# Kernel optimization log

Hardware: AMD Instinct MI355X
Metric: run time of the kernel (lower is better)

The kernel has to match this reference:

```python
import jax, jax.numpy as jnp
import numpy as np

EPS = 1e-4

def _softmax_kernel(data, projection_matrix, is_query):
    # data: [..., n, d], projection_matrix: [m, d]
    d = data.shape[-1]
    m = projection_matrix.shape[0]
    data_normalizer = 1.0 / (d ** 0.25)
    ratio = 1.0 / (m ** 0.5)
    # [..., n, m]
    data_dash = jnp.einsum('...id,jd->...ij', data_normalizer * data, projection_matrix)
    # ||x||^2 / 2 * normalizer^2, shape [..., n, 1]
    diag_data = (jnp.sum(data * data, axis=-1) * 0.5 * data_normalizer ** 2)[..., None]
    if is_query:
        stab = jnp.max(data_dash, axis=-1, keepdims=True)
    else:
        stab = jnp.max(data_dash)
    return ratio * (jnp.exp(data_dash - diag_data - stab) + EPS)

def _linear_attention(q, k, v):
    # q,k: [..., n, m] feature maps; v: [..., n, e]
    D_inv = 1.0 / jnp.einsum('...nd,...d->...n', q, k.sum(axis=-2))
    context = jnp.einsum('...nd,...ne->...de', k, v)  # [..., m, e]
    return jnp.einsum('...de,...nd,...n->...ne', context, q, D_inv)

def setup_inputs() -> dict:
    key = jax.random.key(0)
    k1, k2, k3, k4 = jax.random.split(key, 4)
    B, H, N, D, M = 8, 8, 4096, 64, 266
    return {
        'q': jax.random.normal(k1, (B, H, N, D), dtype=jnp.float32),
        'k': jax.random.normal(k2, (B, H, N, D), dtype=jnp.float32),
        'v': jax.random.normal(k3, (B, H, N, D), dtype=jnp.float32),
        'projection_matrix': jax.random.normal(k4, (M, D), dtype=jnp.float32),
    }

def reference(q, k, v, projection_matrix):
    q_prime = _softmax_kernel(q, projection_matrix, is_query=True)
    k_prime = _softmax_kernel(k, projection_matrix, is_query=False)
    return _linear_attention(q_prime, k_prime, v)
```

## Files before the change

### kernel.cpp

```cpp
#include <hip/hip_runtime.h>
#include <math.h>

#define BH    64
#define NSEQ  4096
#define DDIM  64
#define MDIM  266
#define MPAD  272
#define KTS   40
#define QTS   296
#define RATIO 0.06131393394849658f
#define NORMF 0.35355339059327373f
#define DIAGF 0.0625f
#define EPSF  1e-4f

typedef __attribute__((ext_vector_type(8))) short bf16x8;
typedef __attribute__((ext_vector_type(4))) float f32x4;

__device__ __forceinline__ unsigned fenc(float f) {
  unsigned u = __float_as_uint(f);
  return (u & 0x80000000u) ? ~u : (u | 0x80000000u);
}
__device__ __forceinline__ float fdec(unsigned u) {
  return (u & 0x80000000u) ? __uint_as_float(u & 0x7fffffffu) : __uint_as_float(~u);
}

__device__ __forceinline__ void split1(float x, unsigned short& h, unsigned short& l) {
  unsigned ux = __float_as_uint(x);
  float hf = __uint_as_float(ux & 0xffff0000u);
  h = (unsigned short)(ux >> 16);
  l = (unsigned short)(__float_as_uint(x - hf) >> 16);
}

__device__ __forceinline__ void splitf(float4 a, float4 b, bf16x8& hi, bf16x8& lo) {
  float x[8] = {a.x, a.y, a.z, a.w, b.x, b.y, b.z, b.w};
#pragma unroll
  for (int e = 0; e < 8; ++e) {
    unsigned short h, l;
    split1(x[e], h, l);
    hi[e] = (short)h;
    lo[e] = (short)l;
  }
}

__device__ __forceinline__ f32x4 mfma3(bf16x8 ah, bf16x8 al, bf16x8 bh, bf16x8 bl, f32x4 acc) {
  acc = __builtin_amdgcn_mfma_f32_16x16x32_bf16(ah, bh, acc, 0, 0, 0);
  acc = __builtin_amdgcn_mfma_f32_16x16x32_bf16(ah, bl, acc, 0, 0, 0);
  acc = __builtin_amdgcn_mfma_f32_16x16x32_bf16(al, bh, acc, 0, 0, 0);
  return acc;
}

__global__ __launch_bounds__(256) void pprep_kernel(const float* __restrict__ proj,
                                                    short* __restrict__ phi,
                                                    short* __restrict__ plo) {
  int idx = blockIdx.x * 256 + threadIdx.x;
  if (idx >= MPAD * DDIM) return;
  int j = idx >> 6;
  float x = (j < MDIM) ? proj[idx] : 0.f;
  unsigned short h, l;
  split1(x, h, l);
  phi[idx] = (short)h;
  plo[idx] = (short)l;
}

__global__ __launch_bounds__(256) void kmax_kernel(const float* __restrict__ k,
                                                   const short* __restrict__ phi,
                                                   const short* __restrict__ plo,
                                                   unsigned* __restrict__ kmax) {
  __shared__ float sK[64 * 76];
  __shared__ float wmax[4];
  const int tid = threadIdx.x;
  const int lane = tid & 63, wv = tid >> 6, lrow = lane & 15, lgrp = lane >> 4;

  float tmax = -1e30f;
  for (int it = 0; it < 8; ++it) {
    const int chunk = blockIdx.x * 8 + it;
    const int bh = chunk >> 6, ch = chunk & 63;
    const float* kb = k + ((size_t)bh * NSEQ + (size_t)ch * 64) * DDIM;
    __syncthreads();
#pragma unroll
    for (int t = 0; t < 4; ++t) {
      int fid = tid + t * 256, r = fid >> 4, d4 = fid & 15;
      *(float4*)&sK[r * 76 + d4 * 4] = ((const float4*)kb)[fid];
    }
    __syncthreads();

    bf16x8 ahi[2], alo[2];
#pragma unroll
    for (int s = 0; s < 2; ++s) {
      const float* p = &sK[(wv * 16 + lrow) * 76 + s * 32 + lgrp * 8];
      splitf(*(const float4*)p, *(const float4*)(p + 4), ahi[s], alo[s]);
    }

#pragma unroll
    for (int jt = 0; jt < 17; ++jt) {
      f32x4 acc = {0.f, 0.f, 0.f, 0.f};
#pragma unroll
      for (int s = 0; s < 2; ++s) {
        const size_t bo = ((size_t)(jt * 16 + lrow)) * DDIM + s * 32 + lgrp * 8;
        acc = mfma3(ahi[s], alo[s], *(const bf16x8*)(phi + bo), *(const bf16x8*)(plo + bo), acc);
      }
      if (jt < 16 || lrow < 10) {
#pragma unroll
        for (int i = 0; i < 4; ++i) tmax = fmaxf(tmax, acc[i]);
      }
    }
  }
#pragma unroll
  for (int off = 32; off; off >>= 1) tmax = fmaxf(tmax, __shfl_xor(tmax, off));
  if (lane == 0) wmax[wv] = tmax;
  __syncthreads();
  if (tid == 0) {
    float m = fmaxf(fmaxf(wmax[0], wmax[1]), fmaxf(wmax[2], wmax[3]));
    atomicMax(kmax, fenc(m * NORMF));
  }
}

__device__ __forceinline__ float dash_reg(int jt, const bf16x8* ahi, const bf16x8* alo,
                                          const bf16x8* ph, const bf16x8* pl,
                                          const float* sDiag, float stab,
                                          unsigned short* kThi, unsigned short* kTlo,
                                          int lrow, int lgrp) {
  float kssum = 0.f;
  const int jg = jt * 16 + lrow;
#pragma unroll
  for (int m = 0; m < 2; ++m) {
    f32x4 d = {0.f, 0.f, 0.f, 0.f};
#pragma unroll
    for (int s = 0; s < 2; ++s)
      d = mfma3(ahi[m * 2 + s], alo[m * 2 + s], ph[s], pl[s], d);
    ushort4 h4, l4;
#pragma unroll
    for (int i = 0; i < 4; ++i) {
      const int nl = m * 16 + lgrp * 4 + i;
      float kd = d[i] * NORMF;
      float kp = (jg < MDIM) ? RATIO * (__expf(kd - sDiag[nl] - stab) + EPSF) : 0.f;
      kssum += kp;
      unsigned short h, l;
      split1(kp, h, l);
      ((unsigned short*)&h4)[i] = h;
      ((unsigned short*)&l4)[i] = l;
    }
    *(ushort4*)&kThi[(size_t)jg * KTS + m * 16 + lgrp * 4] = h4;
    *(ushort4*)&kTlo[(size_t)jg * KTS + m * 16 + lgrp * 4] = l4;
  }
  return kssum;
}

__global__ __launch_bounds__(256, 2) void ctx_kernel(const float* __restrict__ k,
                                                     const float* __restrict__ v,
                                                     const short* __restrict__ phi,
                                                     const short* __restrict__ plo,
                                                     const unsigned* __restrict__ kmaxp,
                                                     float* __restrict__ ctxp,
                                                     float* __restrict__ ksump) {
  __shared__ unsigned short kThi[MPAD * KTS];
  __shared__ unsigned short kTlo[MPAD * KTS];
  __shared__ float sV[32 * 68];
  __shared__ float sDiag[32];
  float* sK = (float*)kThi;

  const int tid = threadIdx.x;
  const int lane = tid & 63, wv = tid >> 6, lrow = lane & 15, lgrp = lane >> 4;
  const int bh = blockIdx.x & 63, c8 = blockIdx.x >> 6;
  const float stab = fdec(*kmaxp);
  const float* kb = k + ((size_t)bh * NSEQ + (size_t)c8 * 512) * DDIM;
  const float* vb = v + ((size_t)bh * NSEQ + (size_t)c8 * 512) * DDIM;

  bf16x8 pfh[4][2], pfl[4][2];
#pragma unroll
  for (int t = 0; t < 4; ++t)
#pragma unroll
    for (int s = 0; s < 2; ++s) {
      const size_t bo = ((size_t)((t * 4 + wv) * 16 + lrow)) * DDIM + s * 32 + lgrp * 8;
      pfh[t][s] = *(const bf16x8*)(phi + bo);
      pfl[t][s] = *(const bf16x8*)(plo + bo);
    }
  bf16x8 pfh4[2], pfl4[2];
  if (wv == 0) {
#pragma unroll
    for (int s = 0; s < 2; ++s) {
      const size_t bo = ((size_t)(256 + lrow)) * DDIM + s * 32 + lgrp * 8;
      pfh4[s] = *(const bf16x8*)(phi + bo);
      pfl4[s] = *(const bf16x8*)(plo + bo);
    }
  }

  f32x4 acc[17];
#pragma unroll
  for (int jt = 0; jt < 17; ++jt) acc[jt] = (f32x4){0.f, 0.f, 0.f, 0.f};
  float ks[5] = {0.f, 0.f, 0.f, 0.f, 0.f};

  for (int rt = 0; rt < 16; ++rt) {
#pragma unroll
    for (int t = 0; t < 2; ++t) {
      int fid = tid + t * 256, r = fid >> 4, d4 = fid & 15;
      *(float4*)&sK[r * 76 + d4 * 4] = ((const float4*)(kb + (size_t)rt * 32 * DDIM))[fid];
      *(float4*)&sV[r * 68 + d4 * 4] = ((const float4*)(vb + (size_t)rt * 32 * DDIM))[fid];
    }
    __syncthreads();
    if (tid < 32) {
      float s = 0.f;
      const float* row = &sK[tid * 76];
#pragma unroll
      for (int d = 0; d < 64; d += 4) {
        float4 x = *(const float4*)(row + d);
        s = fmaf(x.x, x.x, fmaf(x.y, x.y, fmaf(x.z, x.z, fmaf(x.w, x.w, s))));
      }
      sDiag[tid] = s * DIAGF;
    }
    bf16x8 ahi[4], alo[4];
#pragma unroll
    for (int m = 0; m < 2; ++m)
#pragma unroll
      for (int s = 0; s < 2; ++s) {
        const float* p = &sK[(m * 16 + lrow) * 76 + s * 32 + lgrp * 8];
        splitf(*(const float4*)p, *(const float4*)(p + 4), ahi[m * 2 + s], alo[m * 2 + s]);
      }
    bf16x8 vbh, vbl;
    {
      float tv[8];
#pragma unroll
      for (int q = 0; q < 8; ++q) tv[q] = sV[(lgrp * 8 + q) * 68 + wv * 16 + lrow];
      splitf(make_float4(tv[0], tv[1], tv[2], tv[3]),
             make_float4(tv[4], tv[5], tv[6], tv[7]), vbh, vbl);
    }
    __syncthreads();

#pragma unroll
    for (int t = 0; t < 4; ++t)
      ks[t] += dash_reg(t * 4 + wv, ahi, alo, pfh[t], pfl[t], sDiag, stab,
                        kThi, kTlo, lrow, lgrp);
    if (wv == 0)
      ks[4] += dash_reg(16, ahi, alo, pfh4, pfl4, sDiag, stab, kThi, kTlo, lrow, lgrp);
    __syncthreads();

#pragma unroll
    for (int jt = 0; jt < 17; ++jt) {
      bf16x8 ah = *(const bf16x8*)&kThi[(size_t)(jt * 16 + lrow) * KTS + lgrp * 8];
      bf16x8 al = *(const bf16x8*)&kTlo[(size_t)(jt * 16 + lrow) * KTS + lgrp * 8];
      acc[jt] = mfma3(ah, al, vbh, vbl, acc[jt]);
    }
    __syncthreads();
  }

  float* ksb = ksump + (size_t)(c8 * BH + bh) * MPAD;
#pragma unroll
  for (int t = 0; t < 4; ++t) {
    float s = ks[t];
    s += __shfl_xor(s, 16);
    s += __shfl_xor(s, 32);
    if (lgrp == 0) ksb[(t * 4 + wv) * 16 + lrow] = s;
  }
  if (wv == 0) {
    float s = ks[4];
    s += __shfl_xor(s, 16);
    s += __shfl_xor(s, 32);
    if (lgrp == 0) ksb[256 + lrow] = s;
  }
  float* cxb = ctxp + (size_t)(c8 * BH + bh) * MPAD * DDIM;
#pragma unroll
  for (int jt = 0; jt < 17; ++jt)
#pragma unroll
    for (int i = 0; i < 4; ++i)
      cxb[(size_t)(jt * 16 + lgrp * 4 + i) * DDIM + wv * 16 + lrow] = acc[jt][i];
}

__global__ __launch_bounds__(256) void reduce_kernel(const float* __restrict__ ctxp,
                                                     const float* __restrict__ ksump,
                                                     float* __restrict__ ctx,
                                                     float* __restrict__ ksum) {
  const size_t SL = (size_t)BH * MPAD * DDIM;
  const int gid = blockIdx.x * 256 + threadIdx.x;
  if (gid < (int)(SL / 4)) {
    float4 s = make_float4(0.f, 0.f, 0.f, 0.f);
#pragma unroll
    for (int c = 0; c < 8; ++c) {
      float4 x = ((const float4*)ctxp)[c * (SL / 4) + gid];
      s.x += x.x; s.y += x.y; s.z += x.z; s.w += x.w;
    }
    ((float4*)ctx)[gid] = s;
  }
  if (gid < BH * MPAD) {
    float s = 0.f;
#pragma unroll
    for (int c = 0; c < 8; ++c) s += ksump[(size_t)c * BH * MPAD + gid];
    ksum[gid] = s;
  }
}

__global__ __launch_bounds__(256, 2) void out_kernel(const float* __restrict__ q,
                                                     const short* __restrict__ phi,
                                                     const short* __restrict__ plo,
                                                     const float* __restrict__ ctx,
                                                     const float* __restrict__ ksum,
                                                     float* __restrict__ out) {
  __shared__ unsigned short qThi[32 * QTS];
  __shared__ unsigned short qTlo[32 * QTS];
  __shared__ float sQ[32 * 76];
  __shared__ float sKs[MPAD];
  __shared__ float sDiag[32];
  __shared__ float sMax[4 * 32];
  __shared__ float sSum[4 * 32];
  const int tid = threadIdx.x;
  const int lane = tid & 63, wv = tid >> 6, lrow = lane & 15, lgrp = lane >> 4;
  const int bh = blockIdx.x & 63, c8 = blockIdx.x >> 6;
  const float* qb = q + ((size_t)bh * NSEQ + (size_t)c8 * 512) * DDIM;

  for (int idx = tid; idx < 512; idx += 256) {
    const int r = idx >> 4, cc = 272 + (idx & 15);
    qThi[r * QTS + cc] = 0;
    qTlo[r * QTS + cc] = 0;
  }
  for (int t = tid; t < MPAD; t += 256) sKs[t] = ksum[(size_t)bh * MPAD + t];

  bf16x8 cbh[9], cbl[9];
#pragma unroll
  for (int kst = 0; kst < 9; ++kst) {
    float tv[8];
#pragma unroll
    for (int qq = 0; qq < 8; ++qq) {
      const int j = kst * 32 + lgrp * 8 + qq;
      tv[qq] = (j < MPAD) ? ctx[((size_t)bh * MPAD + j) * DDIM + wv * 16 + lrow] : 0.f;
    }
    splitf(make_float4(tv[0], tv[1], tv[2], tv[3]),
           make_float4(tv[4], tv[5], tv[6], tv[7]), cbh[kst], cbl[kst]);
  }

  for (int rt = 0; rt < 16; ++rt) {
    __syncthreads();
#pragma unroll
    for (int t = 0; t < 2; ++t) {
      int fid = tid + t * 256, r = fid >> 4, d4 = fid & 15;
      *(float4*)&sQ[r * 76 + d4 * 4] = ((const float4*)(qb + (size_t)rt * 32 * DDIM))[fid];
    }
    __syncthreads();
    if (tid < 32) {
      float s = 0.f;
      const float* row = &sQ[tid * 76];
#pragma unroll
      for (int d = 0; d < 64; d += 4) {
        float4 x = *(const float4*)(row + d);
        s = fmaf(x.x, x.x, fmaf(x.y, x.y, fmaf(x.z, x.z, fmaf(x.w, x.w, s))));
      }
      sDiag[tid] = s * DIAGF;
    }
    bf16x8 ahi[4], alo[4];
#pragma unroll
    for (int m = 0; m < 2; ++m)
#pragma unroll
      for (int s = 0; s < 2; ++s) {
        const float* p = &sQ[(m * 16 + lrow) * 76 + s * 32 + lgrp * 8];
        splitf(*(const float4*)p, *(const float4*)(p + 4), ahi[m * 2 + s], alo[m * 2 + s]);
      }
    __syncthreads();

    f32x4 qd[4][2];
    f32x4 qd4[2] = {(f32x4){0.f, 0.f, 0.f, 0.f}, (f32x4){0.f, 0.f, 0.f, 0.f}};
#pragma unroll
    for (int t = 0; t < 4; ++t) {
      const int jt = t * 4 + wv;
      const size_t bo = ((size_t)(jt * 16 + lrow)) * DDIM + lgrp * 8;
      bf16x8 ph0 = *(const bf16x8*)(phi + bo);
      bf16x8 pl0 = *(const bf16x8*)(plo + bo);
      bf16x8 ph1 = *(const bf16x8*)(phi + bo + 32);
      bf16x8 pl1 = *(const bf16x8*)(plo + bo + 32);
#pragma unroll
      for (int m = 0; m < 2; ++m) {
        f32x4 d = {0.f, 0.f, 0.f, 0.f};
        d = mfma3(ahi[m * 2 + 0], alo[m * 2 + 0], ph0, pl0, d);
        d = mfma3(ahi[m * 2 + 1], alo[m * 2 + 1], ph1, pl1, d);
        qd[t][m] = d * NORMF;
      }
    }
    if (wv == 0) {
      const size_t bo = ((size_t)(256 + lrow)) * DDIM + lgrp * 8;
      bf16x8 ph0 = *(const bf16x8*)(phi + bo);
      bf16x8 pl0 = *(const bf16x8*)(plo + bo);
      bf16x8 ph1 = *(const bf16x8*)(phi + bo + 32);
      bf16x8 pl1 = *(const bf16x8*)(plo + bo + 32);
#pragma unroll
      for (int m = 0; m < 2; ++m) {
        f32x4 d = {0.f, 0.f, 0.f, 0.f};
        d = mfma3(ahi[m * 2 + 0], alo[m * 2 + 0], ph0, pl0, d);
        d = mfma3(ahi[m * 2 + 1], alo[m * 2 + 1], ph1, pl1, d);
        qd4[m] = d * NORMF;
      }
    }

#pragma unroll
    for (int m = 0; m < 2; ++m)
#pragma unroll
      for (int i = 0; i < 4; ++i) {
        float mx = fmaxf(fmaxf(qd[0][m][i], qd[1][m][i]), fmaxf(qd[2][m][i], qd[3][m][i]));
        if (wv == 0 && lrow < 10) mx = fmaxf(mx, qd4[m][i]);
        mx = fmaxf(mx, __shfl_xor(mx, 1));
        mx = fmaxf(mx, __shfl_xor(mx, 2));
        mx = fmaxf(mx, __shfl_xor(mx, 4));
        mx = fmaxf(mx, __shfl_xor(mx, 8));
        if (lrow == 0) sMax[wv * 32 + m * 16 + lgrp * 4 + i] = mx;
      }
    __syncthreads();

    float mrow[2][4], dgr[2][4], srow[2][4];
#pragma unroll
    for (int m = 0; m < 2; ++m)
#pragma unroll
      for (int i = 0; i < 4; ++i) {
        const int row = m * 16 + lgrp * 4 + i;
        mrow[m][i] = fmaxf(fmaxf(sMax[row], sMax[32 + row]),
                           fmaxf(sMax[64 + row], sMax[96 + row]));
        dgr[m][i] = sDiag[row];
        srow[m][i] = 0.f;
      }
#pragma unroll
    for (int t = 0; t < 4; ++t) {
      const int jg = (t * 4 + wv) * 16 + lrow;
      const float ksj = sKs[jg];
#pragma unroll
      for (int m = 0; m < 2; ++m)
#pragma unroll
        for (int i = 0; i < 4; ++i) {
          float val = RATIO * (__expf(qd[t][m][i] - dgr[m][i] - mrow[m][i]) + EPSF);
          qd[t][m][i] = val;
          srow[m][i] = fmaf(val, ksj, srow[m][i]);
        }
    }
    if (wv == 0) {
      const int jg = 256 + lrow;
      const float ksj = sKs[jg];
#pragma unroll
      for (int m = 0; m < 2; ++m)
#pragma unroll
        for (int i = 0; i < 4; ++i) {
          float val = (jg < MDIM) ? RATIO * (__expf(qd4[m][i] - dgr[m][i] - mrow[m][i]) + EPSF)
                                  : 0.f;
          qd4[m][i] = val;
          srow[m][i] = fmaf(val, ksj, srow[m][i]);
        }
    }
#pragma unroll
    for (int m = 0; m < 2; ++m)
#pragma unroll
      for (int i = 0; i < 4; ++i) {
        float s = srow[m][i];
        s += __shfl_xor(s, 1);
        s += __shfl_xor(s, 2);
        s += __shfl_xor(s, 4);
        s += __shfl_xor(s, 8);
        if (lrow == 0) sSum[wv * 32 + m * 16 + lgrp * 4 + i] = s;
      }
    __syncthreads();

    float di[2][4];
#pragma unroll
    for (int m = 0; m < 2; ++m)
#pragma unroll
      for (int i = 0; i < 4; ++i) {
        const int row = m * 16 + lgrp * 4 + i;
        di[m][i] = 1.0f / (sSum[row] + sSum[32 + row] + sSum[64 + row] + sSum[96 + row]);
      }

#pragma unroll
    for (int t = 0; t < 4; ++t) {
      const int j = (t * 4 + wv) * 16 + lrow;
#pragma unroll
      for (int m = 0; m < 2; ++m)
#pragma unroll
        for (int i = 0; i < 4; ++i) {
          unsigned short h, l;
          split1(qd[t][m][i] * di[m][i], h, l);
          const int n = m * 16 + lgrp * 4 + i;
          qThi[n * QTS + j] = h;
          qTlo[n * QTS + j] = l;
        }
    }
    if (wv == 0) {
      const int j = 256 + lrow;
#pragma unroll
      for (int m = 0; m < 2; ++m)
#pragma unroll
        for (int i = 0; i < 4; ++i) {
          unsigned short h, l;
          split1(qd4[m][i] * di[m][i], h, l);
          const int n = m * 16 + lgrp * 4 + i;
          qThi[n * QTS + j] = h;
          qTlo[n * QTS + j] = l;
        }
    }
    __syncthreads();

#pragma unroll
    for (int mt = 0; mt < 2; ++mt) {
      f32x4 acc = {0.f, 0.f, 0.f, 0.f};
#pragma unroll
      for (int kst = 0; kst < 9; ++kst) {
        bf16x8 ah = *(const bf16x8*)&qThi[(mt * 16 + lrow) * QTS + kst * 32 + lgrp * 8];
        bf16x8 al = *(const bf16x8*)&qTlo[(mt * 16 + lrow) * QTS + kst * 32 + lgrp * 8];
        acc = mfma3(ah, al, cbh[kst], cbl[kst], acc);
      }
#pragma unroll
      for (int i = 0; i < 4; ++i) {
        const int n = rt * 32 + mt * 16 + lgrp * 4 + i;
        out[((size_t)bh * NSEQ + (size_t)c8 * 512 + n) * DDIM + wv * 16 + lrow] = acc[i];
      }
    }
  }
}

extern "C" void kernel_launch(void* const* d_in, const int* in_sizes, int n_in,
                              void* d_out, int out_size, void* d_ws, size_t ws_size,
                              hipStream_t stream) {
  (void)in_sizes; (void)n_in; (void)out_size; (void)ws_size;
  const float* q = (const float*)d_in[0];
  const float* k = (const float*)d_in[1];
  const float* v = (const float*)d_in[2];
  const float* proj = (const float*)d_in[3];
  float* out = (float*)d_out;

  unsigned* kmax = (unsigned*)d_ws;
  float* ctx = (float*)((char*)d_ws + 256);
  float* ksum = ctx + (size_t)BH * MPAD * DDIM;
  short* phi = (short*)(ksum + (size_t)BH * MPAD);
  short* plo = phi + (size_t)MPAD * DDIM;

  const size_t SL = (size_t)BH * MPAD * DDIM;
  float* ctxp = (float*)d_out;
  float* ksump = ctxp + 8 * SL;

  hipMemsetAsync(d_ws, 0, 256, stream);
  pprep_kernel<<<dim3((MPAD * DDIM + 255) / 256), dim3(256), 0, stream>>>(proj, phi, plo);
  kmax_kernel<<<dim3(512), dim3(256), 0, stream>>>(k, phi, plo, kmax);
  ctx_kernel<<<dim3(BH * 8), dim3(256), 0, stream>>>(k, v, phi, plo, kmax, ctxp, ksump);
  reduce_kernel<<<dim3((unsigned)(SL / 4 / 256)), dim3(256), 0, stream>>>(ctxp, ksump, ctx, ksum);
  out_kernel<<<dim3(BH * 8), dim3(256), 0, stream>>>(q, phi, plo, ctx, ksum, out);
}
```

Before: 303.9 us.

## Pre-split context to transposed bf16 hi/lo in reduce and restructure out kernel

The reduce kernel now writes the context as transposed bf16 hi/lo planes, so the output kernel no longer does a strided fp32 gather and split at startup. The output kernel reuses the qT LDS buffer for the staged q tile. It writes the split feature map directly in the exp loop and applies the row normalizer after the MFMA, which removes one barrier and a pass over registers. Grid size doubles to 1024 blocks with half the rows each, and launch bounds rise to 4 waves per SIMD for more occupancy. The trade-off is that context fragments are reloaded from global memory on every row tile, and reduce now does scattered 2-byte stores.

```diff
diff --git a/kernel.cpp b/kernel.cpp
--- a/kernel.cpp
+++ b/kernel.cpp
@@ -267,18 +267,30 @@
 
 __global__ __launch_bounds__(256) void reduce_kernel(const float* __restrict__ ctxp,
                                                      const float* __restrict__ ksump,
-                                                     float* __restrict__ ctx,
+                                                     unsigned short* __restrict__ ctxh,
+                                                     unsigned short* __restrict__ ctxl,
                                                      float* __restrict__ ksum) {
   const size_t SL = (size_t)BH * MPAD * DDIM;
   const int gid = blockIdx.x * 256 + threadIdx.x;
-  if (gid < (int)(SL / 4)) {
+  if (gid < BH * MPAD * 16) {
+    const int e4 = gid & 15;
+    const int j = (gid >> 4) % MPAD;
+    const int bh = (gid >> 4) / MPAD;
+    const size_t base = ((size_t)bh * MPAD + j) * DDIM + e4 * 4;
     float4 s = make_float4(0.f, 0.f, 0.f, 0.f);
 #pragma unroll
     for (int c = 0; c < 8; ++c) {
-      float4 x = ((const float4*)ctxp)[c * (SL / 4) + gid];
+      float4 x = *(const float4*)(ctxp + (size_t)c * SL + base);
       s.x += x.x; s.y += x.y; s.z += x.z; s.w += x.w;
     }
-    ((float4*)ctx)[gid] = s;
+#pragma unroll
+    for (int u = 0; u < 4; ++u) {
+      unsigned short h, l;
+      split1(((const float*)&s)[u], h, l);
+      const size_t to = ((size_t)bh * DDIM + e4 * 4 + u) * MPAD + j;
+      ctxh[to] = h;
+      ctxl[to] = l;
+    }
   }
   if (gid < BH * MPAD) {
     float s = 0.f;
@@ -288,45 +300,30 @@
   }
 }
 
-__global__ __launch_bounds__(256, 2) void out_kernel(const float* __restrict__ q,
+__global__ __launch_bounds__(256, 4) void out_kernel(const float* __restrict__ q,
                                                      const short* __restrict__ phi,
                                                      const short* __restrict__ plo,
-                                                     const float* __restrict__ ctx,
+                                                     const unsigned short* __restrict__ ctxh,
+                                                     const unsigned short* __restrict__ ctxl,
                                                      const float* __restrict__ ksum,
                                                      float* __restrict__ out) {
   __shared__ unsigned short qThi[32 * QTS];
   __shared__ unsigned short qTlo[32 * QTS];
-  __shared__ float sQ[32 * 76];
   __shared__ float sKs[MPAD];
   __shared__ float sDiag[32];
-  __shared__ float sMax[4 * 32];
-  __shared__ float sSum[4 * 32];
+  __shared__ float sMax[128], sSum[128];
+  float* sQ = (float*)qThi;
+
   const int tid = threadIdx.x;
   const int lane = tid & 63, wv = tid >> 6, lrow = lane & 15, lgrp = lane >> 4;
-  const int bh = blockIdx.x & 63, c8 = blockIdx.x >> 6;
-  const float* qb = q + ((size_t)bh * NSEQ + (size_t)c8 * 512) * DDIM;
-
-  for (int idx = tid; idx < 512; idx += 256) {
-    const int r = idx >> 4, cc = 272 + (idx & 15);
-    qThi[r * QTS + cc] = 0;
-    qTlo[r * QTS + cc] = 0;
-  }
+  const int bh = blockIdx.x & 63, c16 = blockIdx.x >> 6;
+  const float* qb = q + ((size_t)bh * NSEQ + (size_t)c16 * 256) * DDIM;
+
   for (int t = tid; t < MPAD; t += 256) sKs[t] = ksum[(size_t)bh * MPAD + t];
-
-  bf16x8 cbh[9], cbl[9];
-#pragma unroll
-  for (int kst = 0; kst < 9; ++kst) {
-    float tv[8];
-#pragma unroll
-    for (int qq = 0; qq < 8; ++qq) {
-      const int j = kst * 32 + lgrp * 8 + qq;
-      tv[qq] = (j < MPAD) ? ctx[((size_t)bh * MPAD + j) * DDIM + wv * 16 + lrow] : 0.f;
-    }
-    splitf(make_float4(tv[0], tv[1], tv[2], tv[3]),
-           make_float4(tv[4], tv[5], tv[6], tv[7]), cbh[kst], cbl[kst]);
-  }
-
-  for (int rt = 0; rt < 16; ++rt) {
+  const unsigned short* cth = ctxh + ((size_t)bh * DDIM + wv * 16 + lrow) * MPAD;
+  const unsigned short* ctl = ctxl + ((size_t)bh * DDIM + wv * 16 + lrow) * MPAD;
+
+  for (int rt = 0; rt < 8; ++rt) {
     __syncthreads();
 #pragma unroll
     for (int t = 0; t < 2; ++t) {
@@ -421,7 +418,11 @@
 #pragma unroll
         for (int i = 0; i < 4; ++i) {
           float val = RATIO * (__expf(qd[t][m][i] - dgr[m][i] - mrow[m][i]) + EPSF);
-          qd[t][m][i] = val;
+          unsigned short h, l;
+          split1(val, h, l);
+          const int n = m * 16 + lgrp * 4 + i;
+          qThi[n * QTS + jg] = h;
+          qTlo[n * QTS + jg] = l;
           srow[m][i] = fmaf(val, ksj, srow[m][i]);
         }
     }
@@ -434,8 +435,22 @@
         for (int i = 0; i < 4; ++i) {
           float val = (jg < MDIM) ? RATIO * (__expf(qd4[m][i] - dgr[m][i] - mrow[m][i]) + EPSF)
                                   : 0.f;
-          qd4[m][i] = val;
+          unsigned short h, l;
+          split1(val, h, l);
+          const int n = m * 16 + lgrp * 4 + i;
+          qThi[n * QTS + jg] = h;
+          qTlo[n * QTS + jg] = l;
           srow[m][i] = fmaf(val, ksj, srow[m][i]);
+        }
+    }
+    if (wv == 1) {
+#pragma unroll
+      for (int m = 0; m < 2; ++m)
+#pragma unroll
+        for (int i = 0; i < 4; ++i) {
+          const int n = m * 16 + lgrp * 4 + i;
+          qThi[n * QTS + 272 + lrow] = 0;
+          qTlo[n * QTS + 272 + lrow] = 0;
         }
     }
 #pragma unroll
@@ -449,60 +464,38 @@
         s += __shfl_xor(s, 8);
         if (lrow == 0) sSum[wv * 32 + m * 16 + lgrp * 4 + i] = s;
       }
-    __syncthreads();
-
-    float di[2][4];
-#pragma unroll
-    for (int m = 0; m < 2; ++m)
-#pragma unroll
-      for (int i = 0; i < 4; ++i) {
-        const int row = m * 16 + lgrp * 4 + i;
-        di[m][i] = 1.0f / (sSum[row] + sSum[32 + row] + sSum[64 + row] + sSum[96 + row]);
-      }
-
-#pragma unroll
-    for (int t = 0; t < 4; ++t) {
-      const int j = (t * 4 + wv) * 16 + lrow;
-#pragma unroll
-      for (int m = 0; m < 2; ++m)
-#pragma unroll
-        for (int i = 0; i < 4; ++i) {
-          unsigned short h, l;
-          split1(qd[t][m][i] * di[m][i], h, l);
-          const int n = m * 16 + lgrp * 4 + i;
-          qThi[n * QTS + j] = h;
-          qTlo[n * QTS + j] = l;
-        }
-    }
-    if (wv == 0) {
-      const int j = 256 + lrow;
-#pragma unroll
-      for (int m = 0; m < 2; ++m)
-#pragma unroll
-        for (int i = 0; i < 4; ++i) {
-          unsigned short h, l;
-          split1(qd4[m][i] * di[m][i], h, l);
-          const int n = m * 16 + lgrp * 4 + i;
-          qThi[n * QTS + j] = h;
-          qTlo[n * QTS + j] = l;
-        }
-    }
-    __syncthreads();
-
-#pragma unroll
-    for (int mt = 0; mt < 2; ++mt) {
-      f32x4 acc = {0.f, 0.f, 0.f, 0.f};
-#pragma unroll
-      for (int kst = 0; kst < 9; ++kst) {
-        bf16x8 ah = *(const bf16x8*)&qThi[(mt * 16 + lrow) * QTS + kst * 32 + lgrp * 8];
-        bf16x8 al = *(const bf16x8*)&qTlo[(mt * 16 + lrow) * QTS + kst * 32 + lgrp * 8];
-        acc = mfma3(ah, al, cbh[kst], cbl[kst], acc);
-      }
-#pragma unroll
-      for (int i = 0; i < 4; ++i) {
-        const int n = rt * 32 + mt * 16 + lgrp * 4 + i;
-        out[((size_t)bh * NSEQ + (size_t)c8 * 512 + n) * DDIM + wv * 16 + lrow] = acc[i];
-      }
+
+    const unsigned short* cthp = cth;
+    const unsigned short* ctlp = ctl;
+    asm volatile("" : "+v"(cthp), "+v"(ctlp));
+    bf16x8 cH[9], cL[9];
+#pragma unroll
+    for (int kst = 0; kst < 9; ++kst) {
+      cH[kst] = *(const bf16x8*)(cthp + kst * 32 + lgrp * 8);
+      cL[kst] = *(const bf16x8*)(ctlp + kst * 32 + lgrp * 8);
+    }
+    __syncthreads();
+
+    f32x4 acc0 = {0.f, 0.f, 0.f, 0.f}, acc1 = {0.f, 0.f, 0.f, 0.f};
+#pragma unroll
+    for (int kst = 0; kst < 9; ++kst) {
+      bf16x8 ah0 = *(const bf16x8*)&qThi[lrow * QTS + kst * 32 + lgrp * 8];
+      bf16x8 al0 = *(const bf16x8*)&qTlo[lrow * QTS + kst * 32 + lgrp * 8];
+      acc0 = mfma3(ah0, al0, cH[kst], cL[kst], acc0);
+      bf16x8 ah1 = *(const bf16x8*)&qThi[(16 + lrow) * QTS + kst * 32 + lgrp * 8];
+      bf16x8 al1 = *(const bf16x8*)&qTlo[(16 + lrow) * QTS + kst * 32 + lgrp * 8];
+      acc1 = mfma3(ah1, al1, cH[kst], cL[kst], acc1);
+    }
+#pragma unroll
+    for (int i = 0; i < 4; ++i) {
+      const int r0 = lgrp * 4 + i;
+      const float d0 = 1.0f / (sSum[r0] + sSum[32 + r0] + sSum[64 + r0] + sSum[96 + r0]);
+      out[((size_t)bh * NSEQ + (size_t)c16 * 256 + rt * 32 + r0) * DDIM + wv * 16 + lrow] =
+          acc0[i] * d0;
+      const int r1 = 16 + lgrp * 4 + i;
+      const float d1 = 1.0f / (sSum[r1] + sSum[32 + r1] + sSum[64 + r1] + sSum[96 + r1]);
+      out[((size_t)bh * NSEQ + (size_t)c16 * 256 + rt * 32 + r1) * DDIM + wv * 16 + lrow] =
+          acc1[i] * d1;
     }
   }
 }
@@ -518,8 +511,9 @@
   float* out = (float*)d_out;
 
   unsigned* kmax = (unsigned*)d_ws;
-  float* ctx = (float*)((char*)d_ws + 256);
-  float* ksum = ctx + (size_t)BH * MPAD * DDIM;
+  unsigned short* ctxh = (unsigned short*)((char*)d_ws + 256);
+  unsigned short* ctxl = ctxh + (size_t)BH * DDIM * MPAD;
+  float* ksum = (float*)(ctxl + (size_t)BH * DDIM * MPAD);
   short* phi = (short*)(ksum + (size_t)BH * MPAD);
   short* plo = phi + (size_t)MPAD * DDIM;
 
@@ -531,6 +525,7 @@
   pprep_kernel<<<dim3((MPAD * DDIM + 255) / 256), dim3(256), 0, stream>>>(proj, phi, plo);
   kmax_kernel<<<dim3(512), dim3(256), 0, stream>>>(k, phi, plo, kmax);
   ctx_kernel<<<dim3(BH * 8), dim3(256), 0, stream>>>(k, v, phi, plo, kmax, ctxp, ksump);
-  reduce_kernel<<<dim3((unsigned)(SL / 4 / 256)), dim3(256), 0, stream>>>(ctxp, ksump, ctx, ksum);
-  out_kernel<<<dim3(BH * 8), dim3(256), 0, stream>>>(q, phi, plo, ctx, ksum, out);
-}
+  reduce_kernel<<<dim3((BH * MPAD * 16 + 255) / 256), dim3(256), 0, stream>>>(ctxp, ksump,
+                                                                              ctxh, ctxl, ksum);
+  out_kernel<<<dim3(BH * 16), dim3(256), 0, stream>>>(q, phi, plo, ctxh, ctxl, ksum, out);
+}
```

Result: slower. 357.7 us (+17.7%).
